# Kernel tuning notes

Measured on AMD Instinct MI355X. Metric: run time of the kernel, lower is better.

## Reference

```python
import jax, jax.numpy as jnp
import numpy as np

D_MODEL = 1024
N_HEADS = 16
HEAD_DIM = D_MODEL // N_HEADS
ROPE_THETA = 10000.0


def setup_inputs() -> dict:
    key = jax.random.key(0)
    ks = jax.random.split(key, 5)
    B, S = 4, 2048
    x = jax.random.normal(ks[0], (B, S, D_MODEL), dtype=jnp.float32)
    Wq = jax.random.normal(ks[1], (D_MODEL, D_MODEL), dtype=jnp.float32) * 0.02
    Wk = jax.random.normal(ks[2], (D_MODEL, D_MODEL), dtype=jnp.float32) * 0.02
    Wv = jax.random.normal(ks[3], (D_MODEL, D_MODEL), dtype=jnp.float32) * 0.02
    Wo = jax.random.normal(ks[4], (D_MODEL, D_MODEL), dtype=jnp.float32) * 0.02
    token_positions = jnp.arange(S, dtype=jnp.int32)
    return {"x": x, "token_positions": token_positions, "Wq": Wq, "Wk": Wk, "Wv": Wv, "Wo": Wo}


def apply_rope(t, positions):
    # t: [B, H, S, Dk]; positions: [S]
    half = HEAD_DIM // 2
    inv_freq = 1.0 / (ROPE_THETA ** (jnp.arange(half, dtype=jnp.float32) * 2.0 / HEAD_DIM))
    angles = positions.astype(jnp.float32)[:, None] * inv_freq[None, :]  # [S, half]
    cos = jnp.cos(angles)[None, None]  # [1,1,S,half]
    sin = jnp.sin(angles)[None, None]
    t_even = t[..., 0::2]
    t_odd = t[..., 1::2]
    rot_even = t_even * cos - t_odd * sin
    rot_odd = t_even * sin + t_odd * cos
    out = jnp.stack([rot_even, rot_odd], axis=-1)  # [B,H,S,half,2]
    return out.reshape(t.shape)


def reference(x, token_positions, Wq, Wk, Wv, Wo):
    B, S, _ = x.shape
    H, Dk = N_HEADS, HEAD_DIM
    # QKV projections, split heads -> [B, H, S, Dk]
    q = (x @ Wq).reshape(B, S, H, Dk).transpose(0, 2, 1, 3)
    k = (x @ Wk).reshape(B, S, H, Dk).transpose(0, 2, 1, 3)
    v = (x @ Wv).reshape(B, S, H, Dk).transpose(0, 2, 1, 3)
    q = apply_rope(q, token_positions)
    k = apply_rope(k, token_positions)
    scale = 1.0 / jnp.sqrt(jnp.asarray(Dk, dtype=x.dtype))
    scores = jnp.einsum('bhqd,bhkd->bhqk', q, k) * scale
    causal = jnp.tril(jnp.ones((S, S), dtype=bool))
    scores = jnp.where(causal[None, None], scores, jnp.asarray(-jnp.inf, dtype=scores.dtype))
    attn = jax.nn.softmax(scores, axis=-1)
    ctx = jnp.einsum('bhqk,bhkd->bhqd', attn, v)  # [B,H,S,Dk]
    ctx = ctx.transpose(0, 2, 1, 3).reshape(B, S, H * Dk)
    return ctx @ Wo
```

## Files before the change

### kernel.cpp

```cpp
#include <hip/hip_runtime.h>

typedef unsigned short u16;
typedef unsigned int   u32;
typedef __bf16  bf16x8 __attribute__((ext_vector_type(8)));
typedef float   f32x4  __attribute__((ext_vector_type(4)));
typedef float   f32x16 __attribute__((ext_vector_type(16)));
typedef u16     u16x4  __attribute__((ext_vector_type(4)));
typedef u16     u16x8  __attribute__((ext_vector_type(8)));
typedef u32     u32x4  __attribute__((ext_vector_type(4)));

#define D_MODEL 1024
#define N_HEADS 16
#define HEAD_DIM 64
#define BATCH 4
#define SEQ 2048
#define MROWS (BATCH*SEQ)

__device__ __forceinline__ u16 f2bf(float f){
  unsigned u = __builtin_bit_cast(unsigned, f);
  u += 0x7fffu + ((u >> 16) & 1u);
  return (u16)(u >> 16);
}
__device__ __forceinline__ float bf2f(u16 h){
  unsigned u = ((unsigned)h) << 16;
  return __builtin_bit_cast(float, u);
}
__device__ __forceinline__ u32 cvtpk(float a, float b){
  u32 r; asm("v_cvt_pk_bf16_f32 %0, %1, %2" : "=v"(r) : "v"(a), "v"(b)); return r;
}
__device__ __forceinline__ void gload_lds16(const u16* g, u16* l){
  __builtin_amdgcn_global_load_lds((const __attribute__((address_space(1))) void*)g,
                                   (__attribute__((address_space(3))) void*)l, 16, 0, 0);
}

__global__ void k_cvt_x(const float* __restrict__ x, u16* __restrict__ xb, int n4){
  int i = blockIdx.x * 256 + threadIdx.x;
  if (i >= n4) return;
  float4 v = reinterpret_cast<const float4*>(x)[i];
  u16x4 o;
  o.x = f2bf(v.x); o.y = f2bf(v.y); o.z = f2bf(v.z); o.w = f2bf(v.w);
  *reinterpret_cast<u16x4*>(xb + (size_t)i * 4) = o;
}

__global__ void k_transpose_w(const float* __restrict__ Wq, const float* __restrict__ Wk,
                              const float* __restrict__ Wv, const float* __restrict__ Wo,
                              u16* __restrict__ wt){
  __shared__ float t[32][33];
  int z = blockIdx.z;
  const float* W = (z==0)?Wq:(z==1)?Wk:(z==2)?Wv:Wo;
  u16* O = wt + (size_t)z * (D_MODEL*(size_t)D_MODEL);
  int n0 = blockIdx.x*32, k0 = blockIdx.y*32;
  int tx = threadIdx.x, ty = threadIdx.y;
  #pragma unroll
  for (int i = ty; i < 32; i += 8) t[i][tx] = W[(size_t)(k0+i)*D_MODEL + n0 + tx];
  __syncthreads();
  #pragma unroll
  for (int i = ty; i < 32; i += 8) O[(size_t)(n0+i)*D_MODEL + k0 + tx] = f2bf(t[tx][i]);
}

__global__ void k_rope_tab(const int* __restrict__ pos, float2* __restrict__ tab){
  int i = blockIdx.x * 256 + threadIdx.x;
  int s = i >> 5, f = i & 31;
  float inv = exp2f(-(float)f * (13.287712379549449f / 32.0f));
  float a = (float)pos[s] * inv;
  float sn, cs;
  sincosf(a, &sn, &cs);
  tab[i] = make_float2(cs, sn);
}

template<int MODE>
__global__ __launch_bounds__(256, 4) void k_gemm2(const u16* __restrict__ A, const u16* __restrict__ Bt,
                                                  const float2* __restrict__ tab,
                                                  u16* __restrict__ qout, u16* __restrict__ kout,
                                                  u16* __restrict__ vout, float* __restrict__ fout){
  __shared__ u16 sA0[128*32], sA1[128*32], sB0[128*32], sB1[128*32];
  const int K = 1024;
  int tid = threadIdx.x, lane = tid & 63, w = tid >> 6;
  int lr = lane & 15, lg = lane >> 4;
  int m0 = blockIdx.x * 128, n0 = blockIdx.y * 128;
  int wm = w >> 1, wn = w & 1;
  int srow = lane >> 2, scol = (lane & 3) * 8;
  const u16* ga = A  + (size_t)(m0 + w*16 + srow)*K + scol;
  const u16* gb = Bt + (size_t)(n0 + w*16 + srow)*K + scol;
  f32x4 acc[4][4] = {};

#define STAGE2(t, sa, sb) \
    gload_lds16(ga + (size_t)(t)*32,         sa + (w*16)*32); \
    gload_lds16(ga + (size_t)(t)*32 + 64*K,  sa + (64 + w*16)*32); \
    gload_lds16(gb + (size_t)(t)*32,         sb + (w*16)*32); \
    gload_lds16(gb + (size_t)(t)*32 + 64*K,  sb + (64 + w*16)*32);

#define COMP2(sa, sb) { \
    bf16x8 af[4], bv[4]; \
    _Pragma("unroll") \
    for (int mi = 0; mi < 4; mi++) \
      af[mi] = *(const bf16x8*)&sa[(wm*64 + mi*16 + lr)*32 + lg*8]; \
    _Pragma("unroll") \
    for (int ni = 0; ni < 4; ni++) \
      bv[ni] = *(const bf16x8*)&sb[(wn*64 + ni*16 + lr)*32 + lg*8]; \
    _Pragma("unroll") \
    for (int mi = 0; mi < 4; mi++){ \
      _Pragma("unroll") \
      for (int ni = 0; ni < 4; ni++) \
        acc[mi][ni] = __builtin_amdgcn_mfma_f32_16x16x32_bf16(af[mi], bv[ni], acc[mi][ni], 0, 0, 0); \
    } }

  STAGE2(0, sA0, sB0);
  __syncthreads();
  for (int t2 = 0; t2 < 16; ++t2){
    int t = t2 * 2;
    STAGE2(t+1, sA1, sB1);
    COMP2(sA0, sB0);
    __syncthreads();
    if (t + 2 < 32){ STAGE2(t+2, sA0, sB0); }
    COMP2(sA1, sB1);
    __syncthreads();
  }
#undef STAGE2
#undef COMP2

  #pragma unroll
  for (int mi = 0; mi < 4; mi++){
    int row = m0 + wm*64 + mi*16 + lg*4;
    #pragma unroll
    for (int ni = 0; ni < 4; ni++){
      int col = n0 + wn*64 + ni*16 + lr;
      f32x4 vv = acc[mi][ni];
      if (MODE == 1){
        #pragma unroll
        for (int r = 0; r < 4; r++)
          fout[(size_t)(row + r)*1024 + col] = vv[r];
      } else {
        int cm = col & 1023;
        int hh = cm >> 6, d = cm & 63;
        const int which = n0 >> 10;
        #pragma unroll
        for (int r = 0; r < 4; r++){
          int rr = row + r;
          int bb = rr >> 11, s = rr & (SEQ-1);
          float val = vv[r];
          if (which < 2){
            float partner = __shfl_xor(val, 1);
            float2 cs = tab[s*32 + (d >> 1)];
            float o = (d & 1) ? (partner*cs.y + val*cs.x) : (val*cs.x - partner*cs.y);
            if (which == 0){
              o *= 0.18033688011112042f;
              qout[(size_t)rr*1024 + cm] = f2bf(o);
            } else {
              kout[(((size_t)(bb*N_HEADS + hh))*SEQ + s)*64 + d] = f2bf(o);
            }
          } else {
            vout[(((size_t)(bb*N_HEADS + hh))*(SEQ/16) + (s >> 4))*1024 + d*16 + (s & 15)] = f2bf(val);
          }
        }
      }
    }
  }
}

__global__ __launch_bounds__(256, 3) void k_attn(const u16* __restrict__ q, const u16* __restrict__ k2,
                                                 const u16* __restrict__ v2, u16* __restrict__ ctx){
  __shared__ u16 kv[2][4096];
  const int lane = threadIdx.x & 63, w = threadIdx.x >> 6;
  const int lq = lane & 31, hl = lane >> 5;
  const int B = blockIdx.x;
  const int bh = B & 63, g = 15 - (B >> 6);
  const int b = bh >> 4, h = bh & 15;
  const int qi = 4*g + w;
  const int q0 = qi * 32;
  const int qmax0 = (4*g + 3) * 32;
  const u16* kglob = k2 + (size_t)bh*SEQ*64;
  const u16* vglob = v2 + (size_t)bh*(SEQ/16)*1024;

  const u16* qr_ = q + (size_t)(b*SEQ + q0 + lq)*D_MODEL + h*HEAD_DIM + hl*8;
  bf16x8 qf0 = *(const bf16x8*)&qr_[0];
  bf16x8 qf1 = *(const bf16x8*)&qr_[16];
  bf16x8 qf2 = *(const bf16x8*)&qr_[32];
  bf16x8 qf3 = *(const bf16x8*)&qr_[48];
  f32x16 acc0 = {}, acc1 = {};
  float m = -3.0e38f, l = 0.f;

  auto STAGE = [&](int bf, int jt){
    const u16* ks = kglob + (size_t)(jt + (w<<3) + (lane>>3))*64 + (((lane&7)^(lane>>3))<<3);
    gload_lds16(ks, &kv[bf][w<<9]);
    const u16* vs = vglob + ((size_t)(jt>>4)<<10) + (w<<9) + (lane<<3);
    gload_lds16(vs, &kv[bf][2048 + (w<<9)]);
  };

  STAGE(0, 0);
  __syncthreads();
  int p = 0;
  for (int j0 = 0; j0 <= qmax0; j0 += 32){
    if (j0 + 32 <= qmax0) STAGE(p^1, j0 + 32);
    if (j0 <= q0){
      const char* kb = (const char*)&kv[p][0];
      bf16x8 kf0 = *(const bf16x8*)(kb + lq*128 + (((0+hl) ^ (lq&7))<<4));
      bf16x8 kf1 = *(const bf16x8*)(kb + lq*128 + (((2+hl) ^ (lq&7))<<4));
      bf16x8 kf2 = *(const bf16x8*)(kb + lq*128 + (((4+hl) ^ (lq&7))<<4));
      bf16x8 kf3 = *(const bf16x8*)(kb + lq*128 + (((6+hl) ^ (lq&7))<<4));
      const char* vb = kb + 4096;
      bf16x8 vf00 = *(const bf16x8*)(vb + lq*32 + hl*16);
      bf16x8 vf01 = *(const bf16x8*)(vb + lq*32 + hl*16 + 1024);
      bf16x8 vf10 = *(const bf16x8*)(vb + lq*32 + hl*16 + 2048);
      bf16x8 vf11 = *(const bf16x8*)(vb + lq*32 + hl*16 + 3072);

      f32x16 S = {};
      S = __builtin_amdgcn_mfma_f32_32x32x16_bf16(kf0, qf0, S, 0, 0, 0);
      S = __builtin_amdgcn_mfma_f32_32x32x16_bf16(kf1, qf1, S, 0, 0, 0);
      S = __builtin_amdgcn_mfma_f32_32x32x16_bf16(kf2, qf2, S, 0, 0, 0);
      S = __builtin_amdgcn_mfma_f32_32x32x16_bf16(kf3, qf3, S, 0, 0, 0);

      if (j0 == q0){
        #pragma unroll
        for (int r = 0; r < 16; ++r){
          int kk = (r & 3) + 8*(r >> 2) + 4*hl;
          if (kk > lq) S[r] = -3.0e38f;
        }
      }
      float a0 = fmaxf(fmaxf(S[0],S[1]),  fmaxf(S[2],S[3]));
      float a1 = fmaxf(fmaxf(S[4],S[5]),  fmaxf(S[6],S[7]));
      float a2 = fmaxf(fmaxf(S[8],S[9]),  fmaxf(S[10],S[11]));
      float a3 = fmaxf(fmaxf(S[12],S[13]),fmaxf(S[14],S[15]));
      float pm = fmaxf(fmaxf(a0,a1), fmaxf(a2,a3));
      pm = fmaxf(pm, __shfl_xor(pm, 32));
      if (__any(pm > m + 8.f)){
        float mn = fmaxf(m, pm);
        float cr = __builtin_amdgcn_exp2f(m - mn);
        l *= cr;
        #pragma unroll
        for (int r = 0; r < 16; ++r){ acc0[r] *= cr; acc1[r] *= cr; }
        m = mn;
      }
      #pragma unroll
      for (int r = 0; r < 16; ++r) S[r] = __builtin_amdgcn_exp2f(S[r] - m);
      float s0_ = (S[0]+S[1]) + (S[2]+S[3]);
      float s1_ = (S[4]+S[5]) + (S[6]+S[7]);
      float s2_ = (S[8]+S[9]) + (S[10]+S[11]);
      float s3_ = (S[12]+S[13]) + (S[14]+S[15]);
      l += (s0_+s1_) + (s2_+s3_);
      u32 g0a = cvtpk(S[0], S[1]),  g0b = cvtpk(S[2], S[3]);
      u32 g1a = cvtpk(S[4], S[5]),  g1b = cvtpk(S[6], S[7]);
      u32 g2a = cvtpk(S[8], S[9]),  g2b = cvtpk(S[10],S[11]);
      u32 g3a = cvtpk(S[12],S[13]), g3b = cvtpk(S[14],S[15]);
      u32 s0a = hl ? g0a : g1a, s0b = hl ? g0b : g1b;
      u32 e0a = (u32)__shfl_xor((int)s0a, 32), e0b = (u32)__shfl_xor((int)s0b, 32);
      u32 m0a = hl ? g1a : g0a, m0b = hl ? g1b : g0b;
      u32 s1a = hl ? g2a : g3a, s1b = hl ? g2b : g3b;
      u32 e1a = (u32)__shfl_xor((int)s1a, 32), e1b = (u32)__shfl_xor((int)s1b, 32);
      u32 m1a = hl ? g3a : g2a, m1b = hl ? g3b : g2b;
      u32x4 A0 = { hl ? e0a : m0a, hl ? e0b : m0b, hl ? m0a : e0a, hl ? m0b : e0b };
      u32x4 A1 = { hl ? e1a : m1a, hl ? e1b : m1b, hl ? m1a : e1a, hl ? m1b : e1b };
      bf16x8 pa0 = __builtin_bit_cast(bf16x8, A0);
      bf16x8 pa1 = __builtin_bit_cast(bf16x8, A1);
      acc0 = __builtin_amdgcn_mfma_f32_32x32x16_bf16(vf00, pa0, acc0, 0, 0, 0);
      acc0 = __builtin_amdgcn_mfma_f32_32x32x16_bf16(vf10, pa1, acc0, 0, 0, 0);
      acc1 = __builtin_amdgcn_mfma_f32_32x32x16_bf16(vf01, pa0, acc1, 0, 0, 0);
      acc1 = __builtin_amdgcn_mfma_f32_32x32x16_bf16(vf11, pa1, acc1, 0, 0, 0);
    }
    __syncthreads();
    p ^= 1;
  }
  l += __shfl_xor(l, 32);
  float inv = __builtin_amdgcn_rcpf(l);
  char* tbc = (char*)kv + w*4096;
  #pragma unroll
  for (int r = 0; r < 16; ++r){
    int d0 = (r & 3) + 8*(r >> 2) + 4*hl;
    *(u16*)(tbc + lq*128 + ((2*d0)      ^ ((lq & 7) << 4))) = f2bf(acc0[r] * inv);
    *(u16*)(tbc + lq*128 + ((2*(d0+32)) ^ ((lq & 7) << 4))) = f2bf(acc1[r] * inv);
  }
  int qr2 = lane >> 1, chb = (lane & 1) * 4;
  u16* cp = ctx + (size_t)(b*SEQ + q0 + qr2)*D_MODEL + h*HEAD_DIM;
  #pragma unroll
  for (int i = 0; i < 4; ++i){
    int ch = chb + i;
    u16x8 vv = *(const u16x8*)(tbc + qr2*128 + 16*(ch ^ (qr2 & 7)));
    *(u16x8*)&cp[ch*8] = vv;
  }
}

extern "C" void kernel_launch(void* const* d_in, const int* in_sizes, int n_in,
                              void* d_out, int out_size, void* d_ws, size_t ws_size,
                              hipStream_t stream){
  const float* x  = (const float*)d_in[0];
  const int*  pos = (const int*)d_in[1];
  const float* Wq = (const float*)d_in[2];
  const float* Wk = (const float*)d_in[3];
  const float* Wv = (const float*)d_in[4];
  const float* Wo = (const float*)d_in[5];
  float* out = (float*)d_out;
  char* ws = (char*)d_ws;
  u16* xb   = (u16*)(ws);
  u16* wt   = (u16*)(ws + 16777216);
  u16* qb   = (u16*)(ws + 25165824);
  u16* kbh  = (u16*)(ws + 41943040);
  u16* vt2  = (u16*)(ws + 58720256);
  float2* tab = (float2*)(ws + 75497472);
  u16* ctxb = xb;

  k_cvt_x<<<(MROWS*D_MODEL/4)/256, 256, 0, stream>>>(x, xb, MROWS*D_MODEL/4);
  k_transpose_w<<<dim3(32,32,4), dim3(32,8), 0, stream>>>(Wq, Wk, Wv, Wo, wt);
  k_rope_tab<<<(SEQ*32)/256, 256, 0, stream>>>(pos, tab);
  k_gemm2<0><<<dim3(64,24), 256, 0, stream>>>(xb, wt, tab, qb, kbh, vt2, nullptr);
  k_attn<<<dim3(1024), 256, 0, stream>>>(qb, kbh, vt2, ctxb);
  k_gemm2<1><<<dim3(64,8), 256, 0, stream>>>(ctxb, wt + 3145728, nullptr, nullptr, nullptr, nullptr, out);
}
```

Before: 184.1 us.

## Triple-buffer GEMM loads with one barrier per step and permute Wq/Wk columns for RoPE

Replaces the double-buffered LDS pipeline with a three-stage ring that keeps two tiles in flight, using a partial vmcnt wait and a single barrier per k-step. Wq and Wk columns are permuted within each head so even and odd RoPE partners end up 32 columns apart. Each lane can then read its partner from its own accumulator (ni^2) instead of using a cross-lane shuffle. The change costs more LDS per block (48KB), which may limit occupancy at 4 blocks per CU, and it relies on the permuted layout staying consistent with the Q/K output indexing.

```diff
diff --git a/kernel.cpp b/kernel.cpp
--- a/kernel.cpp
+++ b/kernel.cpp
@@ -55,7 +55,12 @@
   for (int i = ty; i < 32; i += 8) t[i][tx] = W[(size_t)(k0+i)*D_MODEL + n0 + tx];
   __syncthreads();
   #pragma unroll
-  for (int i = ty; i < 32; i += 8) O[(size_t)(n0+i)*D_MODEL + k0 + tx] = f2bf(t[tx][i]);
+  for (int i = ty; i < 32; i += 8){
+    int n = n0 + i;
+    int np = n;
+    if (z < 2){ int d = n & 63; np = (n & ~63) | ((d & 1) << 5) | (d >> 1); }
+    O[(size_t)np*D_MODEL + k0 + tx] = f2bf(t[tx][i]);
+  }
 }
 
 __global__ void k_rope_tab(const int* __restrict__ pos, float2* __restrict__ tab){
@@ -69,11 +74,11 @@
 }
 
 template<int MODE>
-__global__ __launch_bounds__(256, 4) void k_gemm2(const u16* __restrict__ A, const u16* __restrict__ Bt,
+__global__ __launch_bounds__(256, 4) void k_gemm3(const u16* __restrict__ A, const u16* __restrict__ Bt,
                                                   const float2* __restrict__ tab,
                                                   u16* __restrict__ qout, u16* __restrict__ kout,
                                                   u16* __restrict__ vout, float* __restrict__ fout){
-  __shared__ u16 sA0[128*32], sA1[128*32], sB0[128*32], sB1[128*32];
+  __shared__ u16 sh[3*8192];
   const int K = 1024;
   int tid = threadIdx.x, lane = tid & 63, w = tid >> 6;
   int lr = lane & 15, lg = lane >> 4;
@@ -84,20 +89,20 @@
   const u16* gb = Bt + (size_t)(n0 + w*16 + srow)*K + scol;
   f32x4 acc[4][4] = {};
 
-#define STAGE2(t, sa, sb) \
-    gload_lds16(ga + (size_t)(t)*32,         sa + (w*16)*32); \
-    gload_lds16(ga + (size_t)(t)*32 + 64*K,  sa + (64 + w*16)*32); \
-    gload_lds16(gb + (size_t)(t)*32,         sb + (w*16)*32); \
-    gload_lds16(gb + (size_t)(t)*32 + 64*K,  sb + (64 + w*16)*32);
-
-#define COMP2(sa, sb) { \
+#define STG(off, t) { u16* Sb = sh + (off); \
+    gload_lds16(ga + (size_t)(t)*32,        Sb + w*512); \
+    gload_lds16(ga + (size_t)(t)*32 + 64*K, Sb + 2048 + w*512); \
+    gload_lds16(gb + (size_t)(t)*32,        Sb + 4096 + w*512); \
+    gload_lds16(gb + (size_t)(t)*32 + 64*K, Sb + 6144 + w*512); }
+
+#define CMP(off) { const u16* Sb = sh + (off); \
     bf16x8 af[4], bv[4]; \
     _Pragma("unroll") \
     for (int mi = 0; mi < 4; mi++) \
-      af[mi] = *(const bf16x8*)&sa[(wm*64 + mi*16 + lr)*32 + lg*8]; \
+      af[mi] = *(const bf16x8*)&Sb[(wm*64 + mi*16 + lr)*32 + lg*8]; \
     _Pragma("unroll") \
     for (int ni = 0; ni < 4; ni++) \
-      bv[ni] = *(const bf16x8*)&sb[(wn*64 + ni*16 + lr)*32 + lg*8]; \
+      bv[ni] = *(const bf16x8*)&Sb[4096 + (wn*64 + ni*16 + lr)*32 + lg*8]; \
     _Pragma("unroll") \
     for (int mi = 0; mi < 4; mi++){ \
       _Pragma("unroll") \
@@ -105,20 +110,26 @@
         acc[mi][ni] = __builtin_amdgcn_mfma_f32_16x16x32_bf16(af[mi], bv[ni], acc[mi][ni], 0, 0, 0); \
     } }
 
-  STAGE2(0, sA0, sB0);
-  __syncthreads();
-  for (int t2 = 0; t2 < 16; ++t2){
-    int t = t2 * 2;
-    STAGE2(t+1, sA1, sB1);
-    COMP2(sA0, sB0);
-    __syncthreads();
-    if (t + 2 < 32){ STAGE2(t+2, sA0, sB0); }
-    COMP2(sA1, sB1);
-    __syncthreads();
-  }
-#undef STAGE2
-#undef COMP2
-
+  STG(0, 0)
+  STG(8192, 1)
+  int oc = 0, on = 8192, os = 16384;
+  #pragma unroll 1
+  for (int t = 0; t < 31; ++t){
+    asm volatile("s_waitcnt vmcnt(4) lgkmcnt(0)" ::: "memory");
+    __builtin_amdgcn_s_barrier();
+    __builtin_amdgcn_sched_barrier(0);
+    if (t < 30){ STG(os, t+2) }
+    CMP(oc)
+    int tmp = oc; oc = on; on = os; os = tmp;
+  }
+  asm volatile("s_waitcnt vmcnt(0) lgkmcnt(0)" ::: "memory");
+  __builtin_amdgcn_s_barrier();
+  __builtin_amdgcn_sched_barrier(0);
+  CMP(oc)
+#undef STG
+#undef CMP
+
+  const int which = n0 >> 10;
   #pragma unroll
   for (int mi = 0; mi < 4; mi++){
     int row = m0 + wm*64 + mi*16 + lg*4;
@@ -133,21 +144,22 @@
       } else {
         int cm = col & 1023;
         int hh = cm >> 6, d = cm & 63;
-        const int which = n0 >> 10;
+        f32x4 vp = acc[mi][ni ^ 2];
         #pragma unroll
         for (int r = 0; r < 4; r++){
           int rr = row + r;
           int bb = rr >> 11, s = rr & (SEQ-1);
           float val = vv[r];
           if (which < 2){
-            float partner = __shfl_xor(val, 1);
-            float2 cs = tab[s*32 + (d >> 1)];
-            float o = (d & 1) ? (partner*cs.y + val*cs.x) : (val*cs.x - partner*cs.y);
+            float e = (ni < 2) ? val : vp[r];
+            float o = (ni < 2) ? vp[r] : val;
+            float2 cs = tab[s*32 + ((ni & 1) << 4) + lr];
+            float ov = (ni < 2) ? (e*cs.x - o*cs.y) : (e*cs.y + o*cs.x);
             if (which == 0){
-              o *= 0.18033688011112042f;
-              qout[(size_t)rr*1024 + cm] = f2bf(o);
+              ov *= 0.18033688011112042f;
+              qout[(size_t)rr*1024 + cm] = f2bf(ov);
             } else {
-              kout[(((size_t)(bb*N_HEADS + hh))*SEQ + s)*64 + d] = f2bf(o);
+              kout[(((size_t)(bb*N_HEADS + hh))*SEQ + s)*64 + d] = f2bf(ov);
             }
           } else {
             vout[(((size_t)(bb*N_HEADS + hh))*(SEQ/16) + (s >> 4))*1024 + d*16 + (s & 15)] = f2bf(val);
@@ -301,7 +313,7 @@
   k_cvt_x<<<(MROWS*D_MODEL/4)/256, 256, 0, stream>>>(x, xb, MROWS*D_MODEL/4);
   k_transpose_w<<<dim3(32,32,4), dim3(32,8), 0, stream>>>(Wq, Wk, Wv, Wo, wt);
   k_rope_tab<<<(SEQ*32)/256, 256, 0, stream>>>(pos, tab);
-  k_gemm2<0><<<dim3(64,24), 256, 0, stream>>>(xb, wt, tab, qb, kbh, vt2, nullptr);
+  k_gemm3<0><<<dim3(64,24), 256, 0, stream>>>(xb, wt, tab, qb, kbh, vt2, nullptr);
   k_attn<<<dim3(1024), 256, 0, stream>>>(qb, kbh, vt2, ctxb);
-  k_gemm2<1><<<dim3(64,8), 256, 0, stream>>>(ctxb, wt + 3145728, nullptr, nullptr, nullptr, nullptr, out);
-}
+  k_gemm3<1><<<dim3(64,8), 256, 0, stream>>>(ctxb, wt + 3145728, nullptr, nullptr, nullptr, nullptr, out);
+}
```

After: 185.4 us. Within noise of the previous version (+0.7%).
